# Kernel optimization log

Hardware: AMD Instinct MI355X
Metric: run time of the kernel (lower is better)

The kernel has to match this reference:

```python
import jax, jax.numpy as jnp
import numpy as np

B, T, IN, H = 256, 512, 19, 512  # batch, seq_len, input_size, hidden_size
OUT = 1


def setup_inputs() -> dict:
    key = jax.random.key(0)
    ks = jax.random.split(key, 16)
    std = 1.0 / np.sqrt(H)  # reset_parameters: uniform(-1/sqrt(H), 1/sqrt(H))
    u = lambda k, shape: jax.random.uniform(k, shape, jnp.float32, -std, std)
    return {
        "input": jax.random.normal(ks[0], (B, T, IN), jnp.float32),
        "l1_Wx": u(ks[1], (4 * H, IN)),
        "l1_bx": u(ks[2], (4 * H,)),
        "l1_Wh": u(ks[3], (4 * H, H)),
        "l1_bh": u(ks[4], (4 * H,)),
        "l2_Wx": u(ks[5], (4 * H, H)),
        "l2_bx": u(ks[6], (4 * H,)),
        "l2_Wh": u(ks[7], (4 * H, H)),
        "l2_bh": u(ks[8], (4 * H,)),
        "fc1_W": u(ks[9], (H // 2, H)),
        "fc1_b": u(ks[10], (H // 2,)),
        "fc2_W": u(ks[11], (H // 4, H // 2)),
        "fc2_b": u(ks[12], (H // 4,)),
        "fc3_W": u(ks[13], (OUT, H // 4)),
        "fc3_b": u(ks[14], (OUT,)),
    }


def _lstm_layer(x, Wx, bx, Wh, bh):
    # Precompute the input projection for all timesteps (identical math to
    # per-step xh(input), but one big GEMM). x: [B, T, in] -> pre: [B, T, 4H]
    pre = jnp.einsum('bti,gi->btg', x, Wx) + bx
    h_dim = Wh.shape[1]

    def step(carry, p_t):
        h, c = carry
        gates = p_t + h @ Wh.T + bh  # [B, 4H]
        i, f, g, o = jnp.split(gates, 4, axis=-1)
        c = jax.nn.sigmoid(f) * c + jax.nn.sigmoid(i) * jnp.tanh(g)
        h = jax.nn.sigmoid(o) * jnp.tanh(c)
        return (h, c), h

    h0 = jnp.zeros((x.shape[0], h_dim), x.dtype)
    _, hs = jax.lax.scan(step, (h0, h0), jnp.swapaxes(pre, 0, 1))  # hs: [T, B, H]
    return jnp.swapaxes(hs, 0, 1)  # [B, T, H]


def reference(input, l1_Wx, l1_bx, l1_Wh, l1_bh, l2_Wx, l2_bx, l2_Wh, l2_bh,
              fc1_W, fc1_b, fc2_W, fc2_b, fc3_W, fc3_b):
    h1 = _lstm_layer(input, l1_Wx, l1_bx, l1_Wh, l1_bh)
    h2 = _lstm_layer(h1, l2_Wx, l2_bx, l2_Wh, l2_bh)
    out = h2[:, -1, :]  # last timestep of top layer
    out = jax.nn.relu(out @ fc1_W.T + fc1_b)  # dropout = identity (inference)
    out = jax.nn.relu(out @ fc2_W.T + fc2_b)
    out = out @ fc3_W.T + fc3_b
    return jnp.squeeze(out)  # [B]
```

## Files before the change

### kernel.cpp

```cpp
#include <hip/hip_runtime.h>
#include <hip/hip_cooperative_groups.h>

namespace cg = cooperative_groups;

#define Bb   256
#define Tt   512
#define INx  19
#define Hh   512
#define NWG  256
#define NTHR 512

typedef unsigned int u32;
typedef unsigned long long u64;

__device__ __forceinline__ float sigf(float x) { return 1.0f / (1.0f + __expf(-x)); }
__device__ __forceinline__ float tanhfast(float x) {
    float e = __expf(2.0f * x);
    return 1.0f - 2.0f / (e + 1.0f);
}

union pcast { u64 u; float2 f; };
__device__ __forceinline__ void gstore2(float2* p, float2 v) {
    pcast c; c.f = v;
    __hip_atomic_store((u64*)p, c.u, __ATOMIC_RELAXED, __HIP_MEMORY_SCOPE_AGENT);
}

__device__ __forceinline__ void gbar(u32* flags, int wgid, int tid, u32 phase) {
    __syncthreads();
    if (tid == 0)
        __hip_atomic_store(&flags[wgid], phase, __ATOMIC_RELEASE, __HIP_MEMORY_SCOPE_AGENT);
    if (tid < NWG) {
        const u32* fp = &flags[tid];
        while (__hip_atomic_load(fp, __ATOMIC_RELAXED, __HIP_MEMORY_SCOPE_AGENT) < phase)
            __builtin_amdgcn_s_sleep(2);
    }
    __syncthreads();
    __builtin_amdgcn_fence(__ATOMIC_ACQUIRE, "agent");
}

__device__ __forceinline__ void ldh(const float4* __restrict__ hp, int c,
                                    float4 (&A)[4], float4 (&B)[4]) {
    #pragma unroll
    for (int kk = 0; kk < 4; ++kk) {
        A[kk] = hp[(size_t)(c * 4 + kk) * 128];
        B[kk] = hp[(size_t)(c * 4 + kk) * 128 + 1];
    }
}

__device__ __forceinline__ void fmac(const float4 (&A)[4], const float4 (&B)[4],
                                     const float* __restrict__ wk,
                                     float (&a1)[4][4], float (&ax)[4][4], float (&ah)[4][4]) {
    #pragma unroll
    for (int g = 0; g < 4; ++g) {
        const float4 w1 = *reinterpret_cast<const float4*>(wk + (0 + g) * 528);
        const float4 w2 = *reinterpret_cast<const float4*>(wk + (4 + g) * 528);
        const float4 w3 = *reinterpret_cast<const float4*>(wk + (8 + g) * 528);
        a1[g][0] += A[0].x*w1.x + A[1].x*w1.y + A[2].x*w1.z + A[3].x*w1.w;
        a1[g][1] += A[0].z*w1.x + A[1].z*w1.y + A[2].z*w1.z + A[3].z*w1.w;
        a1[g][2] += B[0].x*w1.x + B[1].x*w1.y + B[2].x*w1.z + B[3].x*w1.w;
        a1[g][3] += B[0].z*w1.x + B[1].z*w1.y + B[2].z*w1.z + B[3].z*w1.w;
        ax[g][0] += A[0].x*w2.x + A[1].x*w2.y + A[2].x*w2.z + A[3].x*w2.w;
        ax[g][1] += A[0].z*w2.x + A[1].z*w2.y + A[2].z*w2.z + A[3].z*w2.w;
        ax[g][2] += B[0].x*w2.x + B[1].x*w2.y + B[2].x*w2.z + B[3].x*w2.w;
        ax[g][3] += B[0].z*w2.x + B[1].z*w2.y + B[2].z*w2.z + B[3].z*w2.w;
        ah[g][0] += A[0].y*w3.x + A[1].y*w3.y + A[2].y*w3.z + A[3].y*w3.w;
        ah[g][1] += A[0].w*w3.x + A[1].w*w3.y + A[2].w*w3.z + A[3].w*w3.w;
        ah[g][2] += B[0].y*w3.x + B[1].y*w3.y + B[2].y*w3.z + B[3].y*w3.w;
        ah[g][3] += B[0].w*w3.x + B[1].w*w3.y + B[2].w*w3.z + B[3].w*w3.w;
    }
}

__global__ void __launch_bounds__(NTHR, 2)
lstm_fused(const float* __restrict__ input,
           const float* __restrict__ l1_Wx, const float* __restrict__ l1_bx,
           const float* __restrict__ l1_Wh, const float* __restrict__ l1_bh,
           const float* __restrict__ l2_Wx, const float* __restrict__ l2_bx,
           const float* __restrict__ l2_Wh, const float* __restrict__ l2_bh,
           const float* __restrict__ fc1_W, const float* __restrict__ fc1_b,
           const float* __restrict__ fc2_W, const float* __restrict__ fc2_b,
           const float* __restrict__ fc3_W, const float* __restrict__ fc3_b,
           float* __restrict__ out, float* __restrict__ ws)
{
    __shared__ float wlds[24 * 528];
    __shared__ float wx1l[8 * 20];
    __shared__ float fcb[Hh + 256 + 128];

    cg::grid_group grid = cg::this_grid();
    const int wgid = blockIdx.x;
    const int jb = wgid * 2;
    const int tid = threadIdx.x;
    const int wid = tid >> 6, lane = tid & 63;
    const int su = wid & 1;
    const int bh = wid >> 1;
    const int kq = lane >> 4;
    const int bg = lane & 15;
    const int bB = bh * 64 + bg * 4;
    const int j  = jb + su;

    float2* PA = (float2*)ws;
    float2* PB = PA + Hh * Bb;
    u32* flags = (u32*)(PB + Hh * Bb);

    if (tid == 0)
        __hip_atomic_store(&flags[wgid], 0u, __ATOMIC_RELAXED, __HIP_MEMORY_SCOPE_AGENT);
    grid.sync();

    for (int idx = tid; idx < 24 * 512; idx += NTHR) {
        const int row = idx >> 9, k = idx & 511;
        const int sru = row >= 12 ? 1 : 0;
        const int rr = row - sru * 12;
        const int m = rr >> 2, g = rr & 3;
        const float* src = (m == 0) ? l1_Wh : (m == 1) ? l2_Wx : l2_Wh;
        wlds[row * 528 + (k >> 7) * 132 + (k & 127)] =
            src[(size_t)(g * Hh + jb + sru) * Hh + k];
    }
    if (tid < 8 * INx) {
        const int r = tid / INx, i = tid - r * INx;
        const int sru = r >> 2, g = r & 3;
        wx1l[r * 20 + i] = l1_Wx[(size_t)(g * Hh + jb + sru) * INx + i];
    }
    float b1r[4], b2r[4];
    #pragma unroll
    for (int g = 0; g < 4; ++g) {
        const int row = g * Hh + j;
        b1r[g] = l1_bx[row] + l1_bh[row];
        b2r[g] = l2_bx[row] + l2_bh[row];
    }
    __syncthreads();

    float c1[4], c2[4];
    #pragma unroll
    for (int b = 0; b < 4; ++b) {
        const float* xr = input + (size_t)(bB + b) * Tt * INx;
        float s[4];
        #pragma unroll
        for (int g = 0; g < 4; ++g) {
            float acc = b1r[g];
            #pragma unroll
            for (int i = 0; i < INx; ++i) acc += xr[i] * wx1l[(su * 4 + g) * 20 + i];
            s[g] = acc;
        }
        c1[b] = sigf(s[0]) * tanhfast(s[2]);
        c2[b] = 0.0f;
        const float h1v = sigf(s[3]) * tanhfast(c1[b]);
        if (kq == 0) gstore2(&PA[(size_t)j * Bb + bB + b], make_float2(h1v, 0.0f));
    }
    gbar(flags, wgid, tid, 1u);

    const float2* Pc = PA; float2* Pn = PB;
    const float* wlane = wlds + su * (12 * 528) + kq * 132;

    for (int t = 0; t < Tt; ++t) {
        const bool doL1 = (t < Tt - 1);

        float a1[4][4], ax[4][4], ah[4][4];
        #pragma unroll
        for (int g = 0; g < 4; ++g)
            #pragma unroll
            for (int b = 0; b < 4; ++b) { a1[g][b] = 0.f; ax[g][b] = 0.f; ah[g][b] = 0.f; }

        const float4* hp = (const float4*)Pc + (size_t)(kq * 128) * 128 + (bB >> 1);

        float4 Ac[4], Bc[4], An[4], Bn[4];
        ldh(hp, 0, Ac, Bc);
        #pragma unroll 1
        for (int c = 0; c < 32; c += 2) {
            ldh(hp, c + 1, An, Bn);
            fmac(Ac, Bc, wlane + c * 4, a1, ax, ah);
            if (c < 30) ldh(hp, c + 2, Ac, Bc);
            fmac(An, Bn, wlane + (c + 1) * 4, a1, ax, ah);
        }

        #pragma unroll
        for (int g = 0; g < 4; ++g) {
            #pragma unroll
            for (int b = 0; b < 4; ++b) {
                float v = a1[g][b]; v += __shfl_xor(v, 16, 64); v += __shfl_xor(v, 32, 64); a1[g][b] = v;
                float w = ax[g][b]; w += __shfl_xor(w, 16, 64); w += __shfl_xor(w, 32, 64); ax[g][b] = w;
                float u = ah[g][b]; u += __shfl_xor(u, 16, 64); u += __shfl_xor(u, 32, 64); ah[g][b] = u;
            }
        }

        #pragma unroll
        for (int b = 0; b < 4; ++b) {
            float s2[4];
            #pragma unroll
            for (int g = 0; g < 4; ++g) s2[g] = ax[g][b] + ah[g][b] + b2r[g];

            float h1v = 0.0f;
            if (doL1) {
                const float* xr = input + ((size_t)(bB + b) * Tt + (t + 1)) * INx;
                float s1[4];
                #pragma unroll
                for (int g = 0; g < 4; ++g) {
                    float acc = a1[g][b] + b1r[g];
                    #pragma unroll
                    for (int i = 0; i < INx; ++i) acc += xr[i] * wx1l[(su * 4 + g) * 20 + i];
                    s1[g] = acc;
                }
                const float ig = sigf(s1[0]), fg = sigf(s1[1]);
                const float gg = tanhfast(s1[2]), og = sigf(s1[3]);
                c1[b] = fg * c1[b] + ig * gg;
                h1v = og * tanhfast(c1[b]);
            }
            const float ig = sigf(s2[0]), fg = sigf(s2[1]);
            const float gg = tanhfast(s2[2]), og = sigf(s2[3]);
            c2[b] = fg * c2[b] + ig * gg;
            const float h2v = og * tanhfast(c2[b]);
            if (kq == 0) gstore2(&Pn[(size_t)j * Bb + bB + b], make_float2(h1v, h2v));
        }

        gbar(flags, wgid, tid, (u32)(t + 2));

        const float2* tp = Pc; Pc = Pn; Pn = (float2*)tp;
    }

    float* hh  = fcb;
    float* a1s = fcb + Hh;
    float* a2s = fcb + Hh + 256;
    hh[tid] = Pc[(size_t)tid * Bb + wgid].y;
    __syncthreads();
    if (tid < 256) {
        float acc = fc1_b[tid];
        const float* wr = fc1_W + (size_t)tid * Hh;
        for (int i = 0; i < Hh; ++i) acc += wr[i] * hh[i];
        a1s[tid] = fmaxf(acc, 0.0f);
    }
    __syncthreads();
    if (tid < 128) {
        float acc = fc2_b[tid];
        const float* wr = fc2_W + (size_t)tid * 256;
        for (int i = 0; i < 256; ++i) acc += wr[i] * a1s[i];
        a2s[tid] = fmaxf(acc, 0.0f);
    }
    __syncthreads();
    if (tid == 0) {
        float acc = fc3_b[0];
        for (int i = 0; i < 128; ++i) acc += fc3_W[i] * a2s[i];
        out[wgid] = acc;
    }
}

extern "C" void kernel_launch(void* const* d_in, const int* in_sizes, int n_in,
                              void* d_out, int out_size, void* d_ws, size_t ws_size,
                              hipStream_t stream)
{
    (void)in_sizes; (void)n_in; (void)out_size; (void)ws_size;

    const float* input = (const float*)d_in[0];
    const float* l1_Wx = (const float*)d_in[1];
    const float* l1_bx = (const float*)d_in[2];
    const float* l1_Wh = (const float*)d_in[3];
    const float* l1_bh = (const float*)d_in[4];
    const float* l2_Wx = (const float*)d_in[5];
    const float* l2_bx = (const float*)d_in[6];
    const float* l2_Wh = (const float*)d_in[7];
    const float* l2_bh = (const float*)d_in[8];
    const float* fc1_W = (const float*)d_in[9];
    const float* fc1_b = (const float*)d_in[10];
    const float* fc2_W = (const float*)d_in[11];
    const float* fc2_b = (const float*)d_in[12];
    const float* fc3_W = (const float*)d_in[13];
    const float* fc3_b = (const float*)d_in[14];
    float* out = (float*)d_out;
    float* ws  = (float*)d_ws;

    void* args[] = {
        &input,
        &l1_Wx, &l1_bx, &l1_Wh, &l1_bh,
        &l2_Wx, &l2_bx, &l2_Wh, &l2_bh,
        &fc1_W, &fc1_b, &fc2_W, &fc2_b, &fc3_W, &fc3_b,
        &out, &ws
    };
    hipLaunchCooperativeKernel((void*)lstm_fused, dim3(NWG), dim3(NTHR), args, 0, stream);
}
```

Before: 30.44 ms.

## Retile LSTM workgroups to four hidden units by half batch and merge layer-2 accumulators

```diff
diff --git a/kernel.cpp b/kernel.cpp
--- a/kernel.cpp
+++ b/kernel.cpp
@@ -10,6 +10,14 @@
 #define NWG  256
 #define NTHR 512
 
+#define WROWS 48
+#define WSTR  528
+#define WLDS_FLOATS (WROWS * WSTR)
+#define WX1_FLOATS  (16 * 20)
+#define FCB_FLOATS  (Hh + 256 + 128)
+#define SMEM_FLOATS (WLDS_FLOATS + WX1_FLOATS + FCB_FLOATS)
+#define SMEM_BYTES  (SMEM_FLOATS * 4)
+
 typedef unsigned int u32;
 typedef unsigned long long u64;
 
@@ -49,24 +57,24 @@
 
 __device__ __forceinline__ void fmac(const float4 (&A)[4], const float4 (&B)[4],
                                      const float* __restrict__ wk,
-                                     float (&a1)[4][4], float (&ax)[4][4], float (&ah)[4][4]) {
+                                     float (&a1)[4][4], float (&a2)[4][4]) {
     #pragma unroll
     for (int g = 0; g < 4; ++g) {
-        const float4 w1 = *reinterpret_cast<const float4*>(wk + (0 + g) * 528);
-        const float4 w2 = *reinterpret_cast<const float4*>(wk + (4 + g) * 528);
-        const float4 w3 = *reinterpret_cast<const float4*>(wk + (8 + g) * 528);
+        const float4 w1 = *reinterpret_cast<const float4*>(wk + (0 + g) * WSTR);
+        const float4 w2 = *reinterpret_cast<const float4*>(wk + (4 + g) * WSTR);
+        const float4 w3 = *reinterpret_cast<const float4*>(wk + (8 + g) * WSTR);
         a1[g][0] += A[0].x*w1.x + A[1].x*w1.y + A[2].x*w1.z + A[3].x*w1.w;
         a1[g][1] += A[0].z*w1.x + A[1].z*w1.y + A[2].z*w1.z + A[3].z*w1.w;
         a1[g][2] += B[0].x*w1.x + B[1].x*w1.y + B[2].x*w1.z + B[3].x*w1.w;
         a1[g][3] += B[0].z*w1.x + B[1].z*w1.y + B[2].z*w1.z + B[3].z*w1.w;
-        ax[g][0] += A[0].x*w2.x + A[1].x*w2.y + A[2].x*w2.z + A[3].x*w2.w;
-        ax[g][1] += A[0].z*w2.x + A[1].z*w2.y + A[2].z*w2.z + A[3].z*w2.w;
-        ax[g][2] += B[0].x*w2.x + B[1].x*w2.y + B[2].x*w2.z + B[3].x*w2.w;
-        ax[g][3] += B[0].z*w2.x + B[1].z*w2.y + B[2].z*w2.z + B[3].z*w2.w;
-        ah[g][0] += A[0].y*w3.x + A[1].y*w3.y + A[2].y*w3.z + A[3].y*w3.w;
-        ah[g][1] += A[0].w*w3.x + A[1].w*w3.y + A[2].w*w3.z + A[3].w*w3.w;
-        ah[g][2] += B[0].y*w3.x + B[1].y*w3.y + B[2].y*w3.z + B[3].y*w3.w;
-        ah[g][3] += B[0].w*w3.x + B[1].w*w3.y + B[2].w*w3.z + B[3].w*w3.w;
+        a2[g][0] += A[0].x*w2.x + A[1].x*w2.y + A[2].x*w2.z + A[3].x*w2.w
+                  + A[0].y*w3.x + A[1].y*w3.y + A[2].y*w3.z + A[3].y*w3.w;
+        a2[g][1] += A[0].z*w2.x + A[1].z*w2.y + A[2].z*w2.z + A[3].z*w2.w
+                  + A[0].w*w3.x + A[1].w*w3.y + A[2].w*w3.z + A[3].w*w3.w;
+        a2[g][2] += B[0].x*w2.x + B[1].x*w2.y + B[2].x*w2.z + B[3].x*w2.w
+                  + B[0].y*w3.x + B[1].y*w3.y + B[2].y*w3.z + B[3].y*w3.w;
+        a2[g][3] += B[0].z*w2.x + B[1].z*w2.y + B[2].z*w2.z + B[3].z*w2.w
+                  + B[0].w*w3.x + B[1].w*w3.y + B[2].w*w3.z + B[3].w*w3.w;
     }
 }
 
@@ -81,43 +89,47 @@
            const float* __restrict__ fc3_W, const float* __restrict__ fc3_b,
            float* __restrict__ out, float* __restrict__ ws)
 {
-    __shared__ float wlds[24 * 528];
-    __shared__ float wx1l[8 * 20];
-    __shared__ float fcb[Hh + 256 + 128];
+    extern __shared__ float smem[];
+    float* wlds = smem;
+    float* wx1l = smem + WLDS_FLOATS;
+    float* fcb  = wx1l + WX1_FLOATS;
 
     cg::grid_group grid = cg::this_grid();
     const int wgid = blockIdx.x;
-    const int jb = wgid * 2;
+    const int ug = wgid >> 1;
+    const int bs = wgid & 1;
+    const int jb = ug * 4;
     const int tid = threadIdx.x;
-    const int wid = tid >> 6, lane = tid & 63;
-    const int su = wid & 1;
-    const int bh = wid >> 1;
+
+    const int wid = __builtin_amdgcn_readfirstlane(tid >> 6);
+    const int su = wid & 3;
+    const int bh = wid >> 2;
+    const int lane = tid & 63;
     const int kq = lane >> 4;
     const int bg = lane & 15;
-    const int bB = bh * 64 + bg * 4;
+    const int bB = bs * 128 + bh * 64 + bg * 4;
     const int j  = jb + su;
 
     float2* PA = (float2*)ws;
-    float2* PB = PA + Hh * Bb;
-    u32* flags = (u32*)(PB + Hh * Bb);
+    float2* PB = PA + (size_t)Hh * Bb;
+    u32* flags = (u32*)(PB + (size_t)Hh * Bb);
 
     if (tid == 0)
         __hip_atomic_store(&flags[wgid], 0u, __ATOMIC_RELAXED, __HIP_MEMORY_SCOPE_AGENT);
     grid.sync();
 
-    for (int idx = tid; idx < 24 * 512; idx += NTHR) {
+    for (int idx = tid; idx < WROWS * Hh; idx += NTHR) {
         const int row = idx >> 9, k = idx & 511;
-        const int sru = row >= 12 ? 1 : 0;
-        const int rr = row - sru * 12;
+        const int u = row / 12, rr = row - u * 12;
         const int m = rr >> 2, g = rr & 3;
         const float* src = (m == 0) ? l1_Wh : (m == 1) ? l2_Wx : l2_Wh;
-        wlds[row * 528 + (k >> 7) * 132 + (k & 127)] =
-            src[(size_t)(g * Hh + jb + sru) * Hh + k];
-    }
-    if (tid < 8 * INx) {
+        wlds[row * WSTR + (k >> 7) * 132 + (k & 127)] =
+            src[(size_t)(g * Hh + jb + u) * Hh + k];
+    }
+    if (tid < 16 * INx) {
         const int r = tid / INx, i = tid - r * INx;
-        const int sru = r >> 2, g = r & 3;
-        wx1l[r * 20 + i] = l1_Wx[(size_t)(g * Hh + jb + sru) * INx + i];
+        const int u = r >> 2, g = r & 3;
+        wx1l[r * 20 + i] = l1_Wx[(size_t)(g * Hh + jb + u) * INx + i];
     }
     float b1r[4], b2r[4];
     #pragma unroll
@@ -128,36 +140,38 @@
     }
     __syncthreads();
 
-    float c1[4], c2[4];
-    #pragma unroll
-    for (int b = 0; b < 4; ++b) {
-        const float* xr = input + (size_t)(bB + b) * Tt * INx;
-        float s[4];
+    const float* wlane = wlds + (su * 12) * WSTR + kq * 132;
+
+    float c1[4] = {0.f, 0.f, 0.f, 0.f}, c2[4] = {0.f, 0.f, 0.f, 0.f};
+    if (kq == 0) {
         #pragma unroll
-        for (int g = 0; g < 4; ++g) {
-            float acc = b1r[g];
-            #pragma unroll
-            for (int i = 0; i < INx; ++i) acc += xr[i] * wx1l[(su * 4 + g) * 20 + i];
-            s[g] = acc;
-        }
-        c1[b] = sigf(s[0]) * tanhfast(s[2]);
-        c2[b] = 0.0f;
-        const float h1v = sigf(s[3]) * tanhfast(c1[b]);
-        if (kq == 0) gstore2(&PA[(size_t)j * Bb + bB + b], make_float2(h1v, 0.0f));
+        for (int b = 0; b < 4; ++b) {
+            const float* xr = input + (size_t)(bB + b) * Tt * INx;
+            float s[4];
+            #pragma unroll
+            for (int g = 0; g < 4; ++g) {
+                float acc = b1r[g];
+                #pragma unroll
+                for (int i = 0; i < INx; ++i) acc += xr[i] * wx1l[(su * 4 + g) * 20 + i];
+                s[g] = acc;
+            }
+            c1[b] = sigf(s[0]) * tanhfast(s[2]);
+            gstore2(&PA[(size_t)j * Bb + bB + b],
+                    make_float2(sigf(s[3]) * tanhfast(c1[b]), 0.f));
+        }
     }
     gbar(flags, wgid, tid, 1u);
 
     const float2* Pc = PA; float2* Pn = PB;
-    const float* wlane = wlds + su * (12 * 528) + kq * 132;
 
     for (int t = 0; t < Tt; ++t) {
         const bool doL1 = (t < Tt - 1);
 
-        float a1[4][4], ax[4][4], ah[4][4];
+        float a1[4][4], a2[4][4];
         #pragma unroll
         for (int g = 0; g < 4; ++g)
             #pragma unroll
-            for (int b = 0; b < 4; ++b) { a1[g][b] = 0.f; ax[g][b] = 0.f; ah[g][b] = 0.f; }
+            for (int b = 0; b < 4; ++b) { a1[g][b] = 0.f; a2[g][b] = 0.f; }
 
         const float4* hp = (const float4*)Pc + (size_t)(kq * 128) * 128 + (bB >> 1);
 
@@ -166,9 +180,9 @@
         #pragma unroll 1
         for (int c = 0; c < 32; c += 2) {
             ldh(hp, c + 1, An, Bn);
-            fmac(Ac, Bc, wlane + c * 4, a1, ax, ah);
+            fmac(Ac, Bc, wlane + (c    ) * 4, a1, a2);
             if (c < 30) ldh(hp, c + 2, Ac, Bc);
-            fmac(An, Bn, wlane + (c + 1) * 4, a1, ax, ah);
+            fmac(An, Bn, wlane + (c + 1) * 4, a1, a2);
         }
 
         #pragma unroll
@@ -176,38 +190,37 @@
             #pragma unroll
             for (int b = 0; b < 4; ++b) {
                 float v = a1[g][b]; v += __shfl_xor(v, 16, 64); v += __shfl_xor(v, 32, 64); a1[g][b] = v;
-                float w = ax[g][b]; w += __shfl_xor(w, 16, 64); w += __shfl_xor(w, 32, 64); ax[g][b] = w;
-                float u = ah[g][b]; u += __shfl_xor(u, 16, 64); u += __shfl_xor(u, 32, 64); ah[g][b] = u;
+                float w = a2[g][b]; w += __shfl_xor(w, 16, 64); w += __shfl_xor(w, 32, 64); a2[g][b] = w;
             }
         }
 
-        #pragma unroll
-        for (int b = 0; b < 4; ++b) {
-            float s2[4];
-            #pragma unroll
-            for (int g = 0; g < 4; ++g) s2[g] = ax[g][b] + ah[g][b] + b2r[g];
-
-            float h1v = 0.0f;
-            if (doL1) {
-                const float* xr = input + ((size_t)(bB + b) * Tt + (t + 1)) * INx;
-                float s1[4];
-                #pragma unroll
-                for (int g = 0; g < 4; ++g) {
-                    float acc = a1[g][b] + b1r[g];
+        if (kq == 0) {
+            #pragma unroll
+            for (int b = 0; b < 4; ++b) {
+                const int bb = bB + b;
+                float h1v = 0.f;
+                if (doL1) {
+                    const float* xr = input + ((size_t)bb * Tt + t + 1) * INx;
+                    float s1[4];
                     #pragma unroll
-                    for (int i = 0; i < INx; ++i) acc += xr[i] * wx1l[(su * 4 + g) * 20 + i];
-                    s1[g] = acc;
+                    for (int g = 0; g < 4; ++g) {
+                        float acc = a1[g][b] + b1r[g];
+                        #pragma unroll
+                        for (int i = 0; i < INx; ++i) acc += xr[i] * wx1l[(su * 4 + g) * 20 + i];
+                        s1[g] = acc;
+                    }
+                    const float ig = sigf(s1[0]), fg = sigf(s1[1]);
+                    const float gg = tanhfast(s1[2]), og = sigf(s1[3]);
+                    c1[b] = fg * c1[b] + ig * gg;
+                    h1v = og * tanhfast(c1[b]);
                 }
-                const float ig = sigf(s1[0]), fg = sigf(s1[1]);
-                const float gg = tanhfast(s1[2]), og = sigf(s1[3]);
-                c1[b] = fg * c1[b] + ig * gg;
-                h1v = og * tanhfast(c1[b]);
+                const float ig = sigf(a2[0][b] + b2r[0]);
+                const float fg = sigf(a2[1][b] + b2r[1]);
+                const float gg = tanhfast(a2[2][b] + b2r[2]);
+                const float og = sigf(a2[3][b] + b2r[3]);
+                c2[b] = fg * c2[b] + ig * gg;
+                gstore2(&Pn[(size_t)j * Bb + bb], make_float2(h1v, og * tanhfast(c2[b])));
             }
-            const float ig = sigf(s2[0]), fg = sigf(s2[1]);
-            const float gg = tanhfast(s2[2]), og = sigf(s2[3]);
-            c2[b] = fg * c2[b] + ig * gg;
-            const float h2v = og * tanhfast(c2[b]);
-            if (kq == 0) gstore2(&Pn[(size_t)j * Bb + bB + b], make_float2(h1v, h2v));
         }
 
         gbar(flags, wgid, tid, (u32)(t + 2));
@@ -265,6 +278,9 @@
     float* out = (float*)d_out;
     float* ws  = (float*)d_ws;
 
+    hipFuncSetAttribute((const void*)lstm_fused,
+                        hipFuncAttributeMaxDynamicSharedMemorySize, SMEM_BYTES);
+
     void* args[] = {
         &input,
         &l1_Wx, &l1_bx, &l1_Wh, &l1_bh,
@@ -272,5 +288,6 @@
         &fc1_W, &fc1_b, &fc2_W, &fc2_b, &fc3_W, &fc3_b,
         &out, &ws
     };
-    hipLaunchCooperativeKernel((void*)lstm_fused, dim3(NWG), dim3(NTHR), args, 0, stream);
-}
+    hipLaunchCooperativeKernel((void*)lstm_fused, dim3(NWG), dim3(NTHR), args,
+                               SMEM_BYTES, stream);
+}
```

Measured after the change: 28.47 ms. 6.5% less time.
